# Kernel optimization log

Measured on AMD Instinct MI355X. Metric: run time of the kernel, lower is better.

The kernel has to match this reference:

```python
import jax, jax.numpy as jnp
import numpy as np

TEN_PI = 10.0 * np.pi

def _normalize(x):
    # Normalize each column to [-1, 1]
    x_min = jnp.min(x, axis=0, keepdims=True)
    x_max = jnp.max(x, axis=0, keepdims=True)
    x_range = x_max - x_min
    x_range = jnp.where(x_range == 0, jnp.ones_like(x_range), x_range)
    return 2.0 * (x - x_min) / x_range - 1.0

def _basis_features(xn):
    # 9 elementwise basis functions, stacked on last axis -> [N, d, 9]
    feats = [
        xn,
        jnp.clip(xn ** 2, -100.0, 100.0),
        jnp.clip(xn ** 3, -100.0, 100.0),
        jnp.exp(jnp.clip(xn, -10.0, 10.0)),
        jnp.log(jnp.abs(xn) + 1.0),
        jnp.sqrt(jnp.abs(xn)),
        jnp.tanh(xn),
        jnp.sin(jnp.clip(xn, -TEN_PI, TEN_PI)),
        jnp.abs(xn),
    ]
    return jnp.stack(feats, axis=-1)

def setup_inputs() -> dict:
    key = jax.random.key(0)
    k1, k2 = jax.random.split(key)
    N, d, K = 1000000, 16, 9
    x = jax.random.normal(k1, (N, d), dtype=jnp.float32)
    weights = jax.random.normal(k2, (K,), dtype=jnp.float32) * 0.1
    bias = jnp.zeros((1,), dtype=jnp.float32)
    return {"x": x, "weights": weights, "bias": bias}

def reference(x, weights, bias):
    xn = _normalize(x)                 # [N, d]
    features = _basis_features(xn)     # [N, d, 9]
    out = jnp.einsum('ndk,k->nd', features, weights)[..., None] + bias  # [N, d, 1]
    return out
```

## Files before the change

kernel.cpp:

```cpp
#include <hip/hip_runtime.h>
#include <stdint.h>

#define NCOL 16
typedef float v4f __attribute__((ext_vector_type(4)));

__device__ __forceinline__ uint32_t fkey(float f) {
    uint32_t u = __float_as_uint(f);
    return (u & 0x80000000u) ? ~u : (u | 0x80000000u);
}
__device__ __forceinline__ float fkey_dec(uint32_t k) {
    uint32_t u = (k & 0x80000000u) ? (k ^ 0x80000000u) : ~k;
    return __uint_as_float(u);
}

__global__ void init_minmax(uint32_t* mm) {
    int t = threadIdx.x;
    if (t < NCOL)            mm[t] = fkey(INFINITY);
    else if (t < 2 * NCOL)   mm[t] = fkey(-INFINITY);
}

__global__ void __launch_bounds__(256) colreduce(const v4f* __restrict__ x,
                                                 uint32_t* __restrict__ mm, int n4) {
    int tid = blockIdx.x * blockDim.x + threadIdx.x;
    int stride = gridDim.x * blockDim.x;
    float mn0 = INFINITY, mn1 = INFINITY, mn2 = INFINITY, mn3 = INFINITY;
    float mx0 = -INFINITY, mx1 = -INFINITY, mx2 = -INFINITY, mx3 = -INFINITY;
    for (int i = tid; i < n4; i += stride) {
        v4f v = x[i];
        mn0 = fminf(mn0, v.x); mx0 = fmaxf(mx0, v.x);
        mn1 = fminf(mn1, v.y); mx1 = fmaxf(mx1, v.y);
        mn2 = fminf(mn2, v.z); mx2 = fmaxf(mx2, v.z);
        mn3 = fminf(mn3, v.w); mx3 = fmaxf(mx3, v.w);
    }
    #pragma unroll
    for (int off = 4; off < 64; off <<= 1) {
        mn0 = fminf(mn0, __shfl_xor(mn0, off)); mx0 = fmaxf(mx0, __shfl_xor(mx0, off));
        mn1 = fminf(mn1, __shfl_xor(mn1, off)); mx1 = fmaxf(mx1, __shfl_xor(mx1, off));
        mn2 = fminf(mn2, __shfl_xor(mn2, off)); mx2 = fmaxf(mx2, __shfl_xor(mx2, off));
        mn3 = fminf(mn3, __shfl_xor(mn3, off)); mx3 = fmaxf(mx3, __shfl_xor(mx3, off));
    }
    __shared__ float smn[4][NCOL], smx[4][NCOL];
    int wave = threadIdx.x >> 6;
    int lane = threadIdx.x & 63;
    if (lane < 4) {
        int g = lane * 4;
        smn[wave][g + 0] = mn0; smx[wave][g + 0] = mx0;
        smn[wave][g + 1] = mn1; smx[wave][g + 1] = mx1;
        smn[wave][g + 2] = mn2; smx[wave][g + 2] = mx2;
        smn[wave][g + 3] = mn3; smx[wave][g + 3] = mx3;
    }
    __syncthreads();
    if (threadIdx.x < NCOL) {
        int c = threadIdx.x;
        float m = fminf(fminf(smn[0][c], smn[1][c]), fminf(smn[2][c], smn[3][c]));
        float M = fmaxf(fmaxf(smx[0][c], smx[1][c]), fmaxf(smx[2][c], smx[3][c]));
        atomicMin(&mm[c], fkey(m));
        atomicMax(&mm[NCOL + c], fkey(M));
    }
}

__device__ __forceinline__ float eval_basis(float xn, const float* w, float b) {
    float ax = fabsf(xn);
    float x2 = xn * xn;
    float x3 = x2 * xn;
    float e  = __expf(xn);
    float e2 = e * e;
    float t  = 1.0f - 2.0f * __frcp_rn(e2 + 1.0f);
    float l  = __logf(ax + 1.0f);
    float sq = __fsqrt_rn(ax);
    float sn = __sinf(xn);
    float r = b;
    r = fmaf(w[0], xn, r);
    r = fmaf(w[1], x2, r);
    r = fmaf(w[2], x3, r);
    r = fmaf(w[3], e,  r);
    r = fmaf(w[4], l,  r);
    r = fmaf(w[5], sq, r);
    r = fmaf(w[6], t,  r);
    r = fmaf(w[7], sn, r);
    r = fmaf(w[8], ax, r);
    return r;
}

__global__ void __launch_bounds__(256) feature_kernel(const v4f* __restrict__ x,
                                                      v4f* __restrict__ out,
                                                      const uint32_t* __restrict__ mm,
                                                      const float* __restrict__ wts,
                                                      const float* __restrict__ bias,
                                                      int n4) {
    __shared__ float s_scale[NCOL], s_off[NCOL], s_w[9];
    if (threadIdx.x < NCOL) {
        float mn = fkey_dec(mm[threadIdx.x]);
        float mx = fkey_dec(mm[NCOL + threadIdx.x]);
        float r = mx - mn;
        if (r == 0.0f) r = 1.0f;
        s_scale[threadIdx.x] = 2.0f / r;
        s_off[threadIdx.x]   = -2.0f * mn / r - 1.0f;
    }
    if (threadIdx.x < 9) s_w[threadIdx.x] = wts[threadIdx.x];
    __syncthreads();

    int tid = blockIdx.x * blockDim.x + threadIdx.x;
    int stride = gridDim.x * blockDim.x;
    int g = (tid & 3) * 4;
    float sc0 = s_scale[g + 0], of0 = s_off[g + 0];
    float sc1 = s_scale[g + 1], of1 = s_off[g + 1];
    float sc2 = s_scale[g + 2], of2 = s_off[g + 2];
    float sc3 = s_scale[g + 3], of3 = s_off[g + 3];
    float w[9];
    #pragma unroll
    for (int k = 0; k < 9; ++k) w[k] = s_w[k];
    float b = bias[0];

    for (int i = tid; i < n4; i += stride) {
        v4f v = x[i];
        v4f o;
        o.x = eval_basis(fmaf(v.x, sc0, of0), w, b);
        o.y = eval_basis(fmaf(v.y, sc1, of1), w, b);
        o.z = eval_basis(fmaf(v.z, sc2, of2), w, b);
        o.w = eval_basis(fmaf(v.w, sc3, of3), w, b);
        __builtin_nontemporal_store(o, &out[i]);
    }
}

extern "C" void kernel_launch(void* const* d_in, const int* in_sizes, int n_in,
                              void* d_out, int out_size, void* d_ws, size_t ws_size,
                              hipStream_t stream) {
    const float* x    = (const float*)d_in[0];
    const float* wts  = (const float*)d_in[1];
    const float* bias = (const float*)d_in[2];
    float* out = (float*)d_out;
    uint32_t* mm = (uint32_t*)d_ws;

    int n  = in_sizes[0];
    int n4 = n / 4;

    init_minmax<<<1, 64, 0, stream>>>(mm);
    colreduce<<<2048, 256, 0, stream>>>((const v4f*)x, mm, n4);
    feature_kernel<<<4096, 256, 0, stream>>>((const v4f*)x, (v4f*)out, mm,
                                             wts, bias, n4);
}
```

Baseline: 149.6 us.

## Fuse min/max reduction and feature evaluation into one persistent kernel with grid barrier

Replaces the three launches (init, column reduce, feature eval) with a single persistent kernel of 1024 blocks. A ticket-based software grid barrier built on a global atomic counter separates the init, reduction and evaluation phases. This removes two kernel launch gaps and lets the second pass over x hit in cache. It relies on all 1024 blocks being co-resident; otherwise the barrier deadlocks.

Result: slower. 238.6 us (+59.5%).

```diff
diff --git a/kernel.cpp b/kernel.cpp
--- a/kernel.cpp
+++ b/kernel.cpp
@@ -2,7 +2,11 @@
 #include <stdint.h>
 
 #define NCOL 16
+#define NB   1024
 typedef float v4f __attribute__((ext_vector_type(4)));
+
+__device__ unsigned long long g_arrive = 0;
+__device__ uint32_t g_mm[2 * NCOL];
 
 __device__ __forceinline__ uint32_t fkey(float f) {
     uint32_t u = __float_as_uint(f);
@@ -13,50 +17,19 @@
     return __uint_as_float(u);
 }
 
-__global__ void init_minmax(uint32_t* mm) {
-    int t = threadIdx.x;
-    if (t < NCOL)            mm[t] = fkey(INFINITY);
-    else if (t < 2 * NCOL)   mm[t] = fkey(-INFINITY);
-}
-
-__global__ void __launch_bounds__(256) colreduce(const v4f* __restrict__ x,
-                                                 uint32_t* __restrict__ mm, int n4) {
-    int tid = blockIdx.x * blockDim.x + threadIdx.x;
-    int stride = gridDim.x * blockDim.x;
-    float mn0 = INFINITY, mn1 = INFINITY, mn2 = INFINITY, mn3 = INFINITY;
-    float mx0 = -INFINITY, mx1 = -INFINITY, mx2 = -INFINITY, mx3 = -INFINITY;
-    for (int i = tid; i < n4; i += stride) {
-        v4f v = x[i];
-        mn0 = fminf(mn0, v.x); mx0 = fmaxf(mx0, v.x);
-        mn1 = fminf(mn1, v.y); mx1 = fmaxf(mx1, v.y);
-        mn2 = fminf(mn2, v.z); mx2 = fmaxf(mx2, v.z);
-        mn3 = fminf(mn3, v.w); mx3 = fmaxf(mx3, v.w);
-    }
-    #pragma unroll
-    for (int off = 4; off < 64; off <<= 1) {
-        mn0 = fminf(mn0, __shfl_xor(mn0, off)); mx0 = fmaxf(mx0, __shfl_xor(mx0, off));
-        mn1 = fminf(mn1, __shfl_xor(mn1, off)); mx1 = fmaxf(mx1, __shfl_xor(mx1, off));
-        mn2 = fminf(mn2, __shfl_xor(mn2, off)); mx2 = fmaxf(mx2, __shfl_xor(mx2, off));
-        mn3 = fminf(mn3, __shfl_xor(mn3, off)); mx3 = fmaxf(mx3, __shfl_xor(mx3, off));
-    }
-    __shared__ float smn[4][NCOL], smx[4][NCOL];
-    int wave = threadIdx.x >> 6;
-    int lane = threadIdx.x & 63;
-    if (lane < 4) {
-        int g = lane * 4;
-        smn[wave][g + 0] = mn0; smx[wave][g + 0] = mx0;
-        smn[wave][g + 1] = mn1; smx[wave][g + 1] = mx1;
-        smn[wave][g + 2] = mn2; smx[wave][g + 2] = mx2;
-        smn[wave][g + 3] = mn3; smx[wave][g + 3] = mx3;
+__device__ __forceinline__ void grid_barrier() {
+    __syncthreads();
+    if (threadIdx.x == 0) {
+        unsigned long long ticket =
+            __hip_atomic_fetch_add(&g_arrive, 1ull, __ATOMIC_ACQ_REL,
+                                   __HIP_MEMORY_SCOPE_AGENT) + 1ull;
+        unsigned long long target = ((ticket + (NB - 1)) / NB) * NB;
+        while (__hip_atomic_load(&g_arrive, __ATOMIC_ACQUIRE,
+                                 __HIP_MEMORY_SCOPE_AGENT) < target) {
+            __builtin_amdgcn_s_sleep(8);
+        }
     }
     __syncthreads();
-    if (threadIdx.x < NCOL) {
-        int c = threadIdx.x;
-        float m = fminf(fminf(smn[0][c], smn[1][c]), fminf(smn[2][c], smn[3][c]));
-        float M = fmaxf(fmaxf(smx[0][c], smx[1][c]), fmaxf(smx[2][c], smx[3][c]));
-        atomicMin(&mm[c], fkey(m));
-        atomicMax(&mm[NCOL + c], fkey(M));
-    }
 }
 
 __device__ __forceinline__ float eval_basis(float xn, const float* w, float b) {
@@ -82,16 +55,63 @@
     return r;
 }
 
-__global__ void __launch_bounds__(256) feature_kernel(const v4f* __restrict__ x,
-                                                      v4f* __restrict__ out,
-                                                      const uint32_t* __restrict__ mm,
-                                                      const float* __restrict__ wts,
-                                                      const float* __restrict__ bias,
-                                                      int n4) {
+__global__ void __launch_bounds__(256, 4) fused_kernel(
+        const v4f* __restrict__ x, v4f* __restrict__ out,
+        const float* __restrict__ wts, const float* __restrict__ bias, int n4) {
+    int tid = blockIdx.x * blockDim.x + threadIdx.x;
+    int stride = NB * 256;
+
+    if (blockIdx.x == 0 && threadIdx.x < 2 * NCOL) {
+        uint32_t v = (threadIdx.x < NCOL) ? fkey(INFINITY) : fkey(-INFINITY);
+        __hip_atomic_store(&g_mm[threadIdx.x], v, __ATOMIC_RELAXED,
+                           __HIP_MEMORY_SCOPE_AGENT);
+    }
+    grid_barrier();
+
+    {
+        float mn0 = INFINITY, mn1 = INFINITY, mn2 = INFINITY, mn3 = INFINITY;
+        float mx0 = -INFINITY, mx1 = -INFINITY, mx2 = -INFINITY, mx3 = -INFINITY;
+        for (int i = tid; i < n4; i += stride) {
+            v4f v = x[i];
+            mn0 = fminf(mn0, v.x); mx0 = fmaxf(mx0, v.x);
+            mn1 = fminf(mn1, v.y); mx1 = fmaxf(mx1, v.y);
+            mn2 = fminf(mn2, v.z); mx2 = fmaxf(mx2, v.z);
+            mn3 = fminf(mn3, v.w); mx3 = fmaxf(mx3, v.w);
+        }
+        #pragma unroll
+        for (int off = 4; off < 64; off <<= 1) {
+            mn0 = fminf(mn0, __shfl_xor(mn0, off)); mx0 = fmaxf(mx0, __shfl_xor(mx0, off));
+            mn1 = fminf(mn1, __shfl_xor(mn1, off)); mx1 = fmaxf(mx1, __shfl_xor(mx1, off));
+            mn2 = fminf(mn2, __shfl_xor(mn2, off)); mx2 = fmaxf(mx2, __shfl_xor(mx2, off));
+            mn3 = fminf(mn3, __shfl_xor(mn3, off)); mx3 = fmaxf(mx3, __shfl_xor(mx3, off));
+        }
+        __shared__ float smn[4][NCOL], smx[4][NCOL];
+        int wave = threadIdx.x >> 6;
+        int lane = threadIdx.x & 63;
+        if (lane < 4) {
+            int g = lane * 4;
+            smn[wave][g + 0] = mn0; smx[wave][g + 0] = mx0;
+            smn[wave][g + 1] = mn1; smx[wave][g + 1] = mx1;
+            smn[wave][g + 2] = mn2; smx[wave][g + 2] = mx2;
+            smn[wave][g + 3] = mn3; smx[wave][g + 3] = mx3;
+        }
+        __syncthreads();
+        if (threadIdx.x < NCOL) {
+            int c = threadIdx.x;
+            float m = fminf(fminf(smn[0][c], smn[1][c]), fminf(smn[2][c], smn[3][c]));
+            float M = fmaxf(fmaxf(smx[0][c], smx[1][c]), fmaxf(smx[2][c], smx[3][c]));
+            atomicMin(&g_mm[c], fkey(m));
+            atomicMax(&g_mm[NCOL + c], fkey(M));
+        }
+    }
+    grid_barrier();
+
     __shared__ float s_scale[NCOL], s_off[NCOL], s_w[9];
     if (threadIdx.x < NCOL) {
-        float mn = fkey_dec(mm[threadIdx.x]);
-        float mx = fkey_dec(mm[NCOL + threadIdx.x]);
+        float mn = fkey_dec(__hip_atomic_load(&g_mm[threadIdx.x],
+                        __ATOMIC_RELAXED, __HIP_MEMORY_SCOPE_AGENT));
+        float mx = fkey_dec(__hip_atomic_load(&g_mm[NCOL + threadIdx.x],
+                        __ATOMIC_RELAXED, __HIP_MEMORY_SCOPE_AGENT));
         float r = mx - mn;
         if (r == 0.0f) r = 1.0f;
         s_scale[threadIdx.x] = 2.0f / r;
@@ -100,8 +120,6 @@
     if (threadIdx.x < 9) s_w[threadIdx.x] = wts[threadIdx.x];
     __syncthreads();
 
-    int tid = blockIdx.x * blockDim.x + threadIdx.x;
-    int stride = gridDim.x * blockDim.x;
     int g = (tid & 3) * 4;
     float sc0 = s_scale[g + 0], of0 = s_off[g + 0];
     float sc1 = s_scale[g + 1], of1 = s_off[g + 1];
@@ -126,17 +144,13 @@
 extern "C" void kernel_launch(void* const* d_in, const int* in_sizes, int n_in,
                               void* d_out, int out_size, void* d_ws, size_t ws_size,
                               hipStream_t stream) {
-    const float* x    = (const float*)d_in[0];
+    const v4f* x      = (const v4f*)d_in[0];
     const float* wts  = (const float*)d_in[1];
     const float* bias = (const float*)d_in[2];
-    float* out = (float*)d_out;
-    uint32_t* mm = (uint32_t*)d_ws;
+    v4f* out = (v4f*)d_out;
 
     int n  = in_sizes[0];
     int n4 = n / 4;
 
-    init_minmax<<<1, 64, 0, stream>>>(mm);
-    colreduce<<<2048, 256, 0, stream>>>((const v4f*)x, mm, n4);
-    feature_kernel<<<4096, 256, 0, stream>>>((const v4f*)x, (v4f*)out, mm,
-                                             wts, bias, n4);
+    fused_kernel<<<NB, 256, 0, stream>>>(x, out, wts, bias, n4);
 }
```

## Dual-stream min/max reduction, one-element-per-thread feature kernel, memset init

Applied to the files above, without the earlier changes.

The column min/max reduction now walks two halves of the input at once, with separate accumulators, so each thread has two independent loads in flight. The feature kernel drops its grid-stride loop and launches one thread per float4 across a full-size grid. The init kernel is replaced by two hipMemsetAsync calls that write the sentinel keys. The dual-half split is only correct when half of n4 is a multiple of 4 so columns stay aligned, and the odd-tail handling does the same. It also adds an extra memset operation to the stream.

Result: slower. 153.0 us (+2.3%).

```diff
diff --git a/kernel.cpp b/kernel.cpp
--- a/kernel.cpp
+++ b/kernel.cpp
@@ -13,25 +13,38 @@
     return __uint_as_float(u);
 }
 
-__global__ void init_minmax(uint32_t* mm) {
-    int t = threadIdx.x;
-    if (t < NCOL)            mm[t] = fkey(INFINITY);
-    else if (t < 2 * NCOL)   mm[t] = fkey(-INFINITY);
-}
-
 __global__ void __launch_bounds__(256) colreduce(const v4f* __restrict__ x,
                                                  uint32_t* __restrict__ mm, int n4) {
     int tid = blockIdx.x * blockDim.x + threadIdx.x;
     int stride = gridDim.x * blockDim.x;
-    float mn0 = INFINITY, mn1 = INFINITY, mn2 = INFINITY, mn3 = INFINITY;
-    float mx0 = -INFINITY, mx1 = -INFINITY, mx2 = -INFINITY, mx3 = -INFINITY;
-    for (int i = tid; i < n4; i += stride) {
-        v4f v = x[i];
-        mn0 = fminf(mn0, v.x); mx0 = fmaxf(mx0, v.x);
-        mn1 = fminf(mn1, v.y); mx1 = fmaxf(mx1, v.y);
-        mn2 = fminf(mn2, v.z); mx2 = fmaxf(mx2, v.z);
-        mn3 = fminf(mn3, v.w); mx3 = fmaxf(mx3, v.w);
+    int half = n4 >> 1;
+    float amn0 = INFINITY, amn1 = INFINITY, amn2 = INFINITY, amn3 = INFINITY;
+    float amx0 = -INFINITY, amx1 = -INFINITY, amx2 = -INFINITY, amx3 = -INFINITY;
+    float bmn0 = INFINITY, bmn1 = INFINITY, bmn2 = INFINITY, bmn3 = INFINITY;
+    float bmx0 = -INFINITY, bmx1 = -INFINITY, bmx2 = -INFINITY, bmx3 = -INFINITY;
+    for (int i = tid; i < half; i += stride) {
+        v4f a = x[i];
+        v4f b = x[i + half];
+        amn0 = fminf(amn0, a.x); amx0 = fmaxf(amx0, a.x);
+        amn1 = fminf(amn1, a.y); amx1 = fmaxf(amx1, a.y);
+        amn2 = fminf(amn2, a.z); amx2 = fmaxf(amx2, a.z);
+        amn3 = fminf(amn3, a.w); amx3 = fmaxf(amx3, a.w);
+        bmn0 = fminf(bmn0, b.x); bmx0 = fmaxf(bmx0, b.x);
+        bmn1 = fminf(bmn1, b.y); bmx1 = fmaxf(bmx1, b.y);
+        bmn2 = fminf(bmn2, b.z); bmx2 = fmaxf(bmx2, b.z);
+        bmn3 = fminf(bmn3, b.w); bmx3 = fmaxf(bmx3, b.w);
     }
+    if (tid == 0 && (n4 & 1)) {
+        v4f t = x[n4 - 1];
+        amn0 = fminf(amn0, t.x); amx0 = fmaxf(amx0, t.x);
+        amn1 = fminf(amn1, t.y); amx1 = fmaxf(amx1, t.y);
+        amn2 = fminf(amn2, t.z); amx2 = fmaxf(amx2, t.z);
+        amn3 = fminf(amn3, t.w); amx3 = fmaxf(amx3, t.w);
+    }
+    float mn0 = fminf(amn0, bmn0), mx0 = fmaxf(amx0, bmx0);
+    float mn1 = fminf(amn1, bmn1), mx1 = fmaxf(amx1, bmx1);
+    float mn2 = fminf(amn2, bmn2), mx2 = fmaxf(amx2, bmx2);
+    float mn3 = fminf(amn3, bmn3), mx3 = fmaxf(amx3, bmx3);
     #pragma unroll
     for (int off = 4; off < 64; off <<= 1) {
         mn0 = fminf(mn0, __shfl_xor(mn0, off)); mx0 = fmaxf(mx0, __shfl_xor(mx0, off));
@@ -101,7 +114,7 @@
     __syncthreads();
 
     int tid = blockIdx.x * blockDim.x + threadIdx.x;
-    int stride = gridDim.x * blockDim.x;
+    if (tid >= n4) return;
     int g = (tid & 3) * 4;
     float sc0 = s_scale[g + 0], of0 = s_off[g + 0];
     float sc1 = s_scale[g + 1], of1 = s_off[g + 1];
@@ -112,15 +125,13 @@
     for (int k = 0; k < 9; ++k) w[k] = s_w[k];
     float b = bias[0];
 
-    for (int i = tid; i < n4; i += stride) {
-        v4f v = x[i];
-        v4f o;
-        o.x = eval_basis(fmaf(v.x, sc0, of0), w, b);
-        o.y = eval_basis(fmaf(v.y, sc1, of1), w, b);
-        o.z = eval_basis(fmaf(v.z, sc2, of2), w, b);
-        o.w = eval_basis(fmaf(v.w, sc3, of3), w, b);
-        __builtin_nontemporal_store(o, &out[i]);
-    }
+    v4f v = x[tid];
+    v4f o;
+    o.x = eval_basis(fmaf(v.x, sc0, of0), w, b);
+    o.y = eval_basis(fmaf(v.y, sc1, of1), w, b);
+    o.z = eval_basis(fmaf(v.z, sc2, of2), w, b);
+    o.w = eval_basis(fmaf(v.w, sc3, of3), w, b);
+    __builtin_nontemporal_store(o, &out[tid]);
 }
 
 extern "C" void kernel_launch(void* const* d_in, const int* in_sizes, int n_in,
@@ -135,8 +146,11 @@
     int n  = in_sizes[0];
     int n4 = n / 4;
 
-    init_minmax<<<1, 64, 0, stream>>>(mm);
+    hipMemsetAsync(mm, 0xFF, NCOL * sizeof(uint32_t), stream);
+    hipMemsetAsync(mm + NCOL, 0x00, NCOL * sizeof(uint32_t), stream);
+
     colreduce<<<2048, 256, 0, stream>>>((const v4f*)x, mm, n4);
-    feature_kernel<<<4096, 256, 0, stream>>>((const v4f*)x, (v4f*)out, mm,
-                                             wts, bias, n4);
+    int blocks = (n4 + 255) / 256;
+    feature_kernel<<<blocks, 256, 0, stream>>>((const v4f*)x, (v4f*)out, mm,
+                                               wts, bias, n4);
 }
```
